# Kernel optimization log

Hardware: AMD Instinct MI355X
Metric: run time of the kernel (lower is better)

The kernel has to match this reference:

```python
import jax, jax.numpy as jnp
import numpy as np


def setup_inputs() -> dict:
    key = jax.random.key(0)
    ks = jax.random.split(key, 8)
    B, D, S, H, W = 32, 256, 64, 64, 64
    L = H * W
    return {
        "x": jax.random.normal(ks[0], (B, D, L), jnp.float32),
        "H": H,
        "W": W,
        "w_bcdt": jax.random.normal(ks[1], (3 * S, D), jnp.float32) * 0.02,
        "b_bcdt": jnp.zeros((3 * S,), jnp.float32),
        "w_dw": jax.random.normal(ks[2], (3 * S, 1, 3, 3), jnp.float32) * 0.1,
        "b_dw": jnp.zeros((3 * S,), jnp.float32),
        "w_hz": jax.random.normal(ks[3], (2 * D, D), jnp.float32) * 0.02,
        "b_hz": jnp.zeros((2 * D,), jnp.float32),
        "w_out": jax.random.normal(ks[4], (D, D), jnp.float32) * 0.02,
        "b_out": jnp.zeros((D,), jnp.float32),
        "A_param": jax.random.uniform(ks[5], (S,), jnp.float32, minval=1.0, maxval=16.0),
        "D_param": jnp.ones((1,), jnp.float32),
    }


def reference(x, H, W, w_bcdt, b_bcdt, w_dw, b_dw, w_hz, b_hz, w_out, b_out, A_param, D_param):
    batch, d_model, L = x.shape
    S = A_param.shape[0]
    # BCdt_proj: pointwise conv1d -> (B, 3S, L)
    bcdt = jnp.einsum('oc,bcl->bol', w_bcdt, x) + b_bcdt[None, :, None]
    # depthwise 3x3 conv over (H, W)
    x4 = bcdt.reshape(batch, 3 * S, H, W)
    x4 = jax.lax.conv_general_dilated(
        x4, w_dw, window_strides=(1, 1), padding=((1, 1), (1, 1)),
        dimension_numbers=('NCHW', 'OIHW', 'NCHW'), feature_group_count=3 * S,
    ) + b_dw[None, :, None, None]
    bcdt = x4.reshape(batch, 3 * S, L)
    Bm, Cm, dt = jnp.split(bcdt, 3, axis=1)  # each (B, S, L)
    # gating: softmax over sequence dim L
    Aw = jax.nn.softmax(dt + A_param[None, :, None], axis=-1)
    AB = Aw * Bm  # (B, S, L)
    # global state compression: h = x @ AB^T -> (B, d_model, S)
    h = jnp.einsum('bdl,bsl->bds', x, AB)
    # hz_proj (pointwise conv1d over length S)
    hz = jnp.einsum('oc,bcs->bos', w_hz, h) + b_hz[None, :, None]
    h2, z = jnp.split(hz, 2, axis=1)  # each (B, d_inner, S)
    g = h2 * jax.nn.silu(z) + h2 * D_param[0]
    hout = jnp.einsum('oc,bcs->bos', w_out, g) + b_out[None, :, None]  # (B, d_model, S)
    # expand back: y = h @ C -> (B, d_model, L)
    y = jnp.einsum('bds,bsl->bdl', hout, Cm).reshape(batch, d_model, H, W)
    return (y, hout)
```

## Files before the change

### kernel.cpp

```cpp
#include <hip/hip_runtime.h>
#include <math.h>

#define B_  32
#define D_  256
#define L_  4096
#define S_  64
#define C3_ 192

#define YSZ    ((size_t)B_ * D_ * L_)
#define HOUTSZ ((size_t)B_ * D_ * S_)
#define NCHUNK 16

typedef __attribute__((ext_vector_type(8))) short short8;
typedef __attribute__((ext_vector_type(4))) float f32x4;

__device__ __forceinline__ short f2bf(float f) {
    unsigned u = __float_as_uint(f);
    u += 0x7fffu + ((u >> 16) & 1u);
    return (short)(u >> 16);
}

__device__ __forceinline__ short8 ld_cvt8(const float* p) {
    const float4* q = reinterpret_cast<const float4*>(p);
    float4 p0 = q[0], p1 = q[1];
    short8 s;
    s[0] = f2bf(p0.x); s[1] = f2bf(p0.y); s[2] = f2bf(p0.z); s[3] = f2bf(p0.w);
    s[4] = f2bf(p1.x); s[5] = f2bf(p1.y); s[6] = f2bf(p1.z); s[7] = f2bf(p1.w);
    return s;
}

__global__ __launch_bounds__(256) void k1_bcdt_mfma(
    const float* __restrict__ x, const float* __restrict__ w,
    const float* __restrict__ bias, float* __restrict__ out)
{
    __shared__ __align__(16) short A_lds[192][40];
    __shared__ __align__(16) short B_lds[128][40];
    const int l0 = blockIdx.x * 128;
    const int b  = blockIdx.y;
    const int tid  = threadIdx.x;
    const int lane = tid & 63;
    const int wv   = tid >> 6;
    const int lm   = lane & 15;
    const int kg   = lane >> 4;
    const float* xb = x + (size_t)b * D_ * L_;

    f32x4 acc[12][2];
    #pragma unroll
    for (int mi = 0; mi < 12; ++mi)
        #pragma unroll
        for (int nj = 0; nj < 2; ++nj)
            acc[mi][nj] = (f32x4){0.f, 0.f, 0.f, 0.f};

    for (int k0 = 0; k0 < D_; k0 += 32) {
        if (k0) __syncthreads();
        #pragma unroll
        for (int q = 0; q < 3; ++q) {
            int task = q * 256 + tid;
            int o = task >> 2, kk = (task & 3) * 8;
            *(short8*)&A_lds[o][kk] = ld_cvt8(w + (size_t)o * D_ + k0 + kk);
        }
        #pragma unroll
        for (int q = 0; q < 2; ++q) {
            int task = q * 256 + tid;
            int l = task & 127, dg = task >> 7;
            const float* xp = xb + (size_t)(k0 + dg * 8) * L_ + l0 + l;
            short8 s;
            #pragma unroll
            for (int r = 0; r < 8; ++r) s[r] = f2bf(xp[(size_t)r * L_]);
            *(short8*)&B_lds[l][dg * 8] = s;
        }
        __syncthreads();
        short8 bb[2];
        #pragma unroll
        for (int nj = 0; nj < 2; ++nj)
            bb[nj] = *(const short8*)&B_lds[wv * 32 + nj * 16 + lm][kg * 8];
        #pragma unroll
        for (int mi = 0; mi < 12; ++mi) {
            short8 a = *(const short8*)&A_lds[mi * 16 + lm][kg * 8];
            #pragma unroll
            for (int nj = 0; nj < 2; ++nj)
                acc[mi][nj] = __builtin_amdgcn_mfma_f32_16x16x32_bf16(
                    a, bb[nj], acc[mi][nj], 0, 0, 0);
        }
    }
    float* ob = out + (size_t)b * C3_ * L_;
    const int col = l0 + wv * 32 + lm;
    #pragma unroll
    for (int mi = 0; mi < 12; ++mi) {
        #pragma unroll
        for (int r = 0; r < 4; ++r) {
            int o = mi * 16 + kg * 4 + r;
            float bv = bias[o];
            #pragma unroll
            for (int nj = 0; nj < 2; ++nj)
                ob[(size_t)o * L_ + col + nj * 16] = acc[mi][nj][r] + bv;
        }
    }
}

__global__ __launch_bounds__(256) void k2a_conv_cm(
    const float* __restrict__ pre, const float* __restrict__ wdw,
    const float* __restrict__ bdw, float* __restrict__ cm)
{
    __shared__ float sm[66][66];
    const int s = blockIdx.x;
    const int b = blockIdx.y;
    const int c = 64 + s;
    const int tid = threadIdx.x;
    for (int i = tid; i < 66 * 66; i += 256) (&sm[0][0])[i] = 0.f;
    __syncthreads();
    const float* ip = pre + ((size_t)b * C3_ + c) * L_;
    for (int p = tid; p < 4096; p += 256)
        sm[(p >> 6) + 1][(p & 63) + 1] = ip[p];
    __syncthreads();
    const float* wp = wdw + c * 9;
    float w00 = wp[0], w01 = wp[1], w02 = wp[2],
          w10 = wp[3], w11 = wp[4], w12 = wp[5],
          w20 = wp[6], w21 = wp[7], w22 = wp[8];
    float bb = bdw[c];
    float* op = cm + ((size_t)b * S_ + s) * L_;
    for (int p = tid; p < 4096; p += 256) {
        int yy = p >> 6, xx = p & 63;
        op[p] = bb
            + sm[yy][xx] * w00     + sm[yy][xx + 1] * w01     + sm[yy][xx + 2] * w02
            + sm[yy + 1][xx] * w10 + sm[yy + 1][xx + 1] * w11 + sm[yy + 1][xx + 2] * w12
            + sm[yy + 2][xx] * w20 + sm[yy + 2][xx + 1] * w21 + sm[yy + 2][xx + 2] * w22;
    }
}

__global__ __launch_bounds__(256) void k2b_softmax_ab(
    const float* __restrict__ pre, const float* __restrict__ wdw,
    const float* __restrict__ bdw, float* __restrict__ ab)
{
    __shared__ float sm[66][66];
    __shared__ float red[4];
    const int s = blockIdx.x;
    const int b = blockIdx.y;
    const int tid = threadIdx.x;
    for (int i = tid; i < 66 * 66; i += 256) (&sm[0][0])[i] = 0.f;
    __syncthreads();
    const int cd = 128 + s;
    {
        const float* ip = pre + ((size_t)b * C3_ + cd) * L_;
        for (int p = tid; p < 4096; p += 256)
            sm[(p >> 6) + 1][(p & 63) + 1] = ip[p];
    }
    __syncthreads();
    float dt[16];
    {
        const float* wp = wdw + cd * 9;
        float w00 = wp[0], w01 = wp[1], w02 = wp[2],
              w10 = wp[3], w11 = wp[4], w12 = wp[5],
              w20 = wp[6], w21 = wp[7], w22 = wp[8];
        float bb = bdw[cd];
        #pragma unroll
        for (int i = 0; i < 16; ++i) {
            int p = tid + 256 * i;
            int yy = p >> 6, xx = p & 63;
            dt[i] = bb
                + sm[yy][xx] * w00     + sm[yy][xx + 1] * w01     + sm[yy][xx + 2] * w02
                + sm[yy + 1][xx] * w10 + sm[yy + 1][xx + 1] * w11 + sm[yy + 1][xx + 2] * w12
                + sm[yy + 2][xx] * w20 + sm[yy + 2][xx + 1] * w21 + sm[yy + 2][xx + 2] * w22;
        }
    }
    float mx = dt[0];
    #pragma unroll
    for (int i = 1; i < 16; ++i) mx = fmaxf(mx, dt[i]);
    #pragma unroll
    for (int off = 32; off >= 1; off >>= 1) mx = fmaxf(mx, __shfl_xor(mx, off, 64));
    if ((tid & 63) == 0) red[tid >> 6] = mx;
    __syncthreads();
    mx = fmaxf(fmaxf(red[0], red[1]), fmaxf(red[2], red[3]));
    float e[16];
    float lsum = 0.f;
    #pragma unroll
    for (int i = 0; i < 16; ++i) { e[i] = expf(dt[i] - mx); lsum += e[i]; }
    #pragma unroll
    for (int off = 32; off >= 1; off >>= 1) lsum += __shfl_xor(lsum, off, 64);
    __syncthreads();
    if ((tid & 63) == 0) red[tid >> 6] = lsum;
    __syncthreads();
    const float inv = 1.f / (red[0] + red[1] + red[2] + red[3]);
    {
        const float* ip = pre + ((size_t)b * C3_ + s) * L_;
        for (int p = tid; p < 4096; p += 256)
            sm[(p >> 6) + 1][(p & 63) + 1] = ip[p];
    }
    __syncthreads();
    {
        const float* wp = wdw + s * 9;
        float w00 = wp[0], w01 = wp[1], w02 = wp[2],
              w10 = wp[3], w11 = wp[4], w12 = wp[5],
              w20 = wp[6], w21 = wp[7], w22 = wp[8];
        float bb = bdw[s];
        float* op = ab + ((size_t)b * S_ + s) * L_;
        #pragma unroll
        for (int i = 0; i < 16; ++i) {
            int p = tid + 256 * i;
            int yy = p >> 6, xx = p & 63;
            float bm = bb
                + sm[yy][xx] * w00     + sm[yy][xx + 1] * w01     + sm[yy][xx + 2] * w02
                + sm[yy + 1][xx] * w10 + sm[yy + 1][xx + 1] * w11 + sm[yy + 1][xx + 2] * w12
                + sm[yy + 2][xx] * w20 + sm[yy + 2][xx + 1] * w21 + sm[yy + 2][xx + 2] * w22;
            op[p] = e[i] * inv * bm;
        }
    }
}

__global__ __launch_bounds__(256) void k3_hpart_mfma(
    const float* __restrict__ x, const float* __restrict__ ab,
    float* __restrict__ hp)
{
    const int dt    = blockIdx.x;
    const int b     = blockIdx.y;
    const int chunk = blockIdx.z;
    const int tid  = threadIdx.x;
    const int lane = tid & 63;
    const int wv   = tid >> 6;
    const int wr   = wv >> 1, wc = wv & 1;
    const int lm   = lane & 15, kg = lane >> 4;
    const int d_base = dt * 128 + wr * 64;
    const int s_base = wc * 32;
    const float* xb  = x  + (size_t)b * D_ * L_;
    const float* abb = ab + (size_t)b * S_ * L_;

    f32x4 acc[4][2];
    #pragma unroll
    for (int mi = 0; mi < 4; ++mi)
        #pragma unroll
        for (int nj = 0; nj < 2; ++nj)
            acc[mi][nj] = (f32x4){0.f, 0.f, 0.f, 0.f};

    #pragma unroll 2
    for (int ks = 0; ks < 8; ++ks) {
        const int l = chunk * 256 + ks * 32 + kg * 8;
        short8 bfr[2];
        #pragma unroll
        for (int nj = 0; nj < 2; ++nj)
            bfr[nj] = ld_cvt8(abb + (size_t)(s_base + nj * 16 + lm) * L_ + l);
        #pragma unroll
        for (int mi = 0; mi < 4; ++mi) {
            short8 a = ld_cvt8(xb + (size_t)(d_base + mi * 16 + lm) * L_ + l);
            #pragma unroll
            for (int nj = 0; nj < 2; ++nj)
                acc[mi][nj] = __builtin_amdgcn_mfma_f32_16x16x32_bf16(
                    a, bfr[nj], acc[mi][nj], 0, 0, 0);
        }
    }
    float* hpo = hp + (size_t)chunk * HOUTSZ + (size_t)b * D_ * S_;
    #pragma unroll
    for (int mi = 0; mi < 4; ++mi)
        #pragma unroll
        for (int r = 0; r < 4; ++r) {
            int d = d_base + mi * 16 + kg * 4 + r;
            #pragma unroll
            for (int nj = 0; nj < 2; ++nj)
                hpo[(size_t)d * S_ + s_base + nj * 16 + lm] = acc[mi][nj][r];
        }
}

__global__ __launch_bounds__(256) void k3r_reduce(
    const float* __restrict__ hp, float* __restrict__ h)
{
    size_t i = (size_t)blockIdx.x * 256 + threadIdx.x;
    float sum = 0.f;
    #pragma unroll
    for (int c = 0; c < NCHUNK; ++c) sum += hp[(size_t)c * HOUTSZ + i];
    h[i] = sum;
}

__global__ __launch_bounds__(256) void k4a_gate(
    const float* __restrict__ h, const float* __restrict__ whz,
    const float* __restrict__ bhz, const float* __restrict__ Dp,
    float* __restrict__ g)
{
    __shared__ float Ah[16][68];
    __shared__ float Az[16][68];
    __shared__ float Bs[16][64];
    const int o0 = blockIdx.x * 64;
    const int b  = blockIdx.y;
    const int tid = threadIdx.x;
    const int tx = tid & 15, ty = tid >> 4;
    float acch[4][4] = {}, accz[4][4] = {};
    const float* hb = h + (size_t)b * D_ * S_;
    for (int k0 = 0; k0 < D_; k0 += 16) {
        {
            int o = tid & 15, k = tid >> 4;
            #pragma unroll
            for (int i = 0; i < 4; ++i) {
                Ah[k][o + 16 * i] = whz[(size_t)(o0 + o + 16 * i) * D_ + k0 + k];
                Az[k][o + 16 * i] = whz[(size_t)(o0 + o + 16 * i + 256) * D_ + k0 + k];
            }
        }
        {
            int s = tid & 63, k = tid >> 6;
            #pragma unroll
            for (int i = 0; i < 4; ++i)
                Bs[k + 4 * i][s] = hb[(size_t)(k0 + k + 4 * i) * S_ + s];
        }
        __syncthreads();
        #pragma unroll
        for (int k = 0; k < 16; ++k) {
            float ah[4], az[4], bb[4];
            #pragma unroll
            for (int i = 0; i < 4; ++i) { ah[i] = Ah[k][ty * 4 + i]; az[i] = Az[k][ty * 4 + i]; }
            #pragma unroll
            for (int j = 0; j < 4; ++j) bb[j] = Bs[k][tx * 4 + j];
            #pragma unroll
            for (int i = 0; i < 4; ++i)
                #pragma unroll
                for (int j = 0; j < 4; ++j) {
                    acch[i][j] += ah[i] * bb[j];
                    accz[i][j] += az[i] * bb[j];
                }
        }
        __syncthreads();
    }
    const float dp = Dp[0];
    #pragma unroll
    for (int i = 0; i < 4; ++i) {
        int o = o0 + ty * 4 + i;
        float bh = bhz[o], bz = bhz[o + 256];
        #pragma unroll
        for (int j = 0; j < 4; ++j) {
            float h2 = acch[i][j] + bh;
            float z  = accz[i][j] + bz;
            float sil = z / (1.f + expf(-z));
            g[((size_t)b * D_ + o) * S_ + tx * 4 + j] = h2 * (sil + dp);
        }
    }
}

__global__ __launch_bounds__(256) void k4b_hout(
    const float* __restrict__ g, const float* __restrict__ wout,
    const float* __restrict__ bout, float* __restrict__ hout)
{
    __shared__ float At[16][68];
    __shared__ float Bs[16][64];
    const int o0 = blockIdx.x * 64;
    const int b  = blockIdx.y;
    const int tid = threadIdx.x;
    const int tx = tid & 15, ty = tid >> 4;
    float acc[4][4] = {};
    const float* gb = g + (size_t)b * D_ * S_;
    for (int k0 = 0; k0 < D_; k0 += 16) {
        {
            int o = tid & 15, k = tid >> 4;
            #pragma unroll
            for (int i = 0; i < 4; ++i)
                At[k][o + 16 * i] = wout[(size_t)(o0 + o + 16 * i) * D_ + k0 + k];
        }
        {
            int s = tid & 63, k = tid >> 6;
            #pragma unroll
            for (int i = 0; i < 4; ++i)
                Bs[k + 4 * i][s] = gb[(size_t)(k0 + k + 4 * i) * S_ + s];
        }
        __syncthreads();
        #pragma unroll
        for (int k = 0; k < 16; ++k) {
            float a[4], bb[4];
            #pragma unroll
            for (int i = 0; i < 4; ++i) a[i] = At[k][ty * 4 + i];
            #pragma unroll
            for (int j = 0; j < 4; ++j) bb[j] = Bs[k][tx * 4 + j];
            #pragma unroll
            for (int i = 0; i < 4; ++i)
                #pragma unroll
                for (int j = 0; j < 4; ++j)
                    acc[i][j] += a[i] * bb[j];
        }
        __syncthreads();
    }
    #pragma unroll
    for (int i = 0; i < 4; ++i) {
        int o = o0 + ty * 4 + i;
        float bv = bout[o];
        #pragma unroll
        for (int j = 0; j < 4; ++j)
            hout[((size_t)b * D_ + o) * S_ + tx * 4 + j] = acc[i][j] + bv;
    }
}

__global__ __launch_bounds__(256) void k5_expand_mfma(
    const float* __restrict__ hout, const float* __restrict__ cm,
    float* __restrict__ y)
{
    __shared__ __align__(16) short A_lds[64][72];
    __shared__ __align__(16) short B_lds[128][72];
    const int l0 = blockIdx.x * 128;
    const int d0 = blockIdx.y * 64;
    const int b  = blockIdx.z;
    const int tid  = threadIdx.x;
    const int lane = tid & 63;
    const int wv   = tid >> 6;
    const int lm   = lane & 15, kg = lane >> 4;

    #pragma unroll
    for (int q = 0; q < 2; ++q) {
        int task = q * 256 + tid;
        int d = task >> 3, sg = (task & 7) * 8;
        *(short8*)&A_lds[d][sg] = ld_cvt8(hout + ((size_t)b * D_ + d0 + d) * S_ + sg);
    }
    #pragma unroll
    for (int q = 0; q < 4; ++q) {
        int l = tid & 127;
        int sg = (q * 2 + (tid >> 7)) * 8;
        const float* cp = cm + ((size_t)b * S_ + sg) * L_ + l0 + l;
        short8 s;
        #pragma unroll
        for (int r = 0; r < 8; ++r) s[r] = f2bf(cp[(size_t)r * L_]);
        *(short8*)&B_lds[l][sg] = s;
    }
    __syncthreads();

    f32x4 acc[4][2];
    #pragma unroll
    for (int mi = 0; mi < 4; ++mi)
        #pragma unroll
        for (int nj = 0; nj < 2; ++nj)
            acc[mi][nj] = (f32x4){0.f, 0.f, 0.f, 0.f};
    #pragma unroll
    for (int ks = 0; ks < 2; ++ks) {
        short8 bb[2];
        #pragma unroll
        for (int nj = 0; nj < 2; ++nj)
            bb[nj] = *(const short8*)&B_lds[wv * 32 + nj * 16 + lm][ks * 32 + kg * 8];
        #pragma unroll
        for (int mi = 0; mi < 4; ++mi) {
            short8 a = *(const short8*)&A_lds[mi * 16 + lm][ks * 32 + kg * 8];
            #pragma unroll
            for (int nj = 0; nj < 2; ++nj)
                acc[mi][nj] = __builtin_amdgcn_mfma_f32_16x16x32_bf16(
                    a, bb[nj], acc[mi][nj], 0, 0, 0);
        }
    }
    const int col = l0 + wv * 32 + lm;
    #pragma unroll
    for (int mi = 0; mi < 4; ++mi)
        #pragma unroll
        for (int r = 0; r < 4; ++r)
            #pragma unroll
            for (int nj = 0; nj < 2; ++nj)
                y[((size_t)b * D_ + d0 + mi * 16 + kg * 4 + r) * L_ + col + nj * 16]
                    = acc[mi][nj][r];
}

extern "C" void kernel_launch(void* const* d_in, const int* in_sizes, int n_in,
                              void* d_out, int out_size, void* d_ws, size_t ws_size,
                              hipStream_t stream)
{
    const float* x      = (const float*)d_in[0];
    const float* w_bcdt = (const float*)d_in[3];
    const float* b_bcdt = (const float*)d_in[4];
    const float* w_dw   = (const float*)d_in[5];
    const float* b_dw   = (const float*)d_in[6];
    const float* w_hz   = (const float*)d_in[7];
    const float* b_hz   = (const float*)d_in[8];
    const float* w_out  = (const float*)d_in[9];
    const float* b_out  = (const float*)d_in[10];
    const float* Dp     = (const float*)d_in[12];

    float* ws  = (float*)d_ws;
    float* pre = ws;
    float* ab  = ws + 25165824;
    float* cm  = ab + 8388608;
    float* hp  = pre;
    float* h   = pre + 8388608;
    float* g   = pre + 8388608 + 524288;

    float* y    = (float*)d_out;
    float* hout = (float*)d_out + YSZ;

    k1_bcdt_mfma  <<<dim3(32, 32),     256, 0, stream>>>(x, w_bcdt, b_bcdt, pre);
    k2a_conv_cm   <<<dim3(64, 32),     256, 0, stream>>>(pre, w_dw, b_dw, cm);
    k2b_softmax_ab<<<dim3(64, 32),     256, 0, stream>>>(pre, w_dw, b_dw, ab);
    k3_hpart_mfma <<<dim3(2, 32, NCHUNK), 256, 0, stream>>>(x, ab, hp);
    k3r_reduce    <<<2048,             256, 0, stream>>>(hp, h);
    k4a_gate      <<<dim3(4, 32),      256, 0, stream>>>(h, w_hz, b_hz, Dp, g);
    k4b_hout      <<<dim3(4, 32),      256, 0, stream>>>(g, w_out, b_out, hout);
    k5_expand_mfma<<<dim3(32, 4, 32),  256, 0, stream>>>(hout, cm, y);
}
```

Baseline: 256.1 us.

## Store intermediates in bf16, merge conv kernels, fold chunk reduction into gate

The pre-projection, Cm and AB intermediates are now written and read as bf16 instead of fp32, which halves their memory traffic. The downstream MFMA kernels can then load bf16 directly without converting. The two depthwise-conv kernels are merged into one launch that splits by block index. The separate chunk-reduction kernel is removed, and k4a_gate sums the partial results while loading. This costs some precision in the intermediates and adds redundant partial-sum reads inside the gate kernel.

```diff
diff --git a/kernel.cpp b/kernel.cpp
--- a/kernel.cpp
+++ b/kernel.cpp
@@ -13,13 +13,17 @@
 
 typedef __attribute__((ext_vector_type(8))) short short8;
 typedef __attribute__((ext_vector_type(4))) float f32x4;
+typedef unsigned short ushort_t;
+typedef unsigned int uint_t;
 
 __device__ __forceinline__ short f2bf(float f) {
     unsigned u = __float_as_uint(f);
     u += 0x7fffu + ((u >> 16) & 1u);
     return (short)(u >> 16);
 }
-
+__device__ __forceinline__ float bf2f(ushort_t u) {
+    return __uint_as_float((uint_t)u << 16);
+}
 __device__ __forceinline__ short8 ld_cvt8(const float* p) {
     const float4* q = reinterpret_cast<const float4*>(p);
     float4 p0 = q[0], p1 = q[1];
@@ -31,7 +35,7 @@
 
 __global__ __launch_bounds__(256) void k1_bcdt_mfma(
     const float* __restrict__ x, const float* __restrict__ w,
-    const float* __restrict__ bias, float* __restrict__ out)
+    const float* __restrict__ bias, ushort_t* __restrict__ out)
 {
     __shared__ __align__(16) short A_lds[192][40];
     __shared__ __align__(16) short B_lds[128][40];
@@ -83,7 +87,7 @@
                     a, bb[nj], acc[mi][nj], 0, 0, 0);
         }
     }
-    float* ob = out + (size_t)b * C3_ * L_;
+    ushort_t* ob = out + (size_t)b * C3_ * L_;
     const int col = l0 + wv * 32 + lm;
     #pragma unroll
     for (int mi = 0; mi < 12; ++mi) {
@@ -93,57 +97,65 @@
             float bv = bias[o];
             #pragma unroll
             for (int nj = 0; nj < 2; ++nj)
-                ob[(size_t)o * L_ + col + nj * 16] = acc[mi][nj][r] + bv;
-        }
-    }
-}
-
-__global__ __launch_bounds__(256) void k2a_conv_cm(
-    const float* __restrict__ pre, const float* __restrict__ wdw,
-    const float* __restrict__ bdw, float* __restrict__ cm)
-{
-    __shared__ float sm[66][66];
-    const int s = blockIdx.x;
-    const int b = blockIdx.y;
-    const int c = 64 + s;
-    const int tid = threadIdx.x;
-    for (int i = tid; i < 66 * 66; i += 256) (&sm[0][0])[i] = 0.f;
-    __syncthreads();
-    const float* ip = pre + ((size_t)b * C3_ + c) * L_;
-    for (int p = tid; p < 4096; p += 256)
-        sm[(p >> 6) + 1][(p & 63) + 1] = ip[p];
-    __syncthreads();
-    const float* wp = wdw + c * 9;
-    float w00 = wp[0], w01 = wp[1], w02 = wp[2],
-          w10 = wp[3], w11 = wp[4], w12 = wp[5],
-          w20 = wp[6], w21 = wp[7], w22 = wp[8];
-    float bb = bdw[c];
-    float* op = cm + ((size_t)b * S_ + s) * L_;
-    for (int p = tid; p < 4096; p += 256) {
-        int yy = p >> 6, xx = p & 63;
-        op[p] = bb
-            + sm[yy][xx] * w00     + sm[yy][xx + 1] * w01     + sm[yy][xx + 2] * w02
-            + sm[yy + 1][xx] * w10 + sm[yy + 1][xx + 1] * w11 + sm[yy + 1][xx + 2] * w12
-            + sm[yy + 2][xx] * w20 + sm[yy + 2][xx + 1] * w21 + sm[yy + 2][xx + 2] * w22;
-    }
-}
-
-__global__ __launch_bounds__(256) void k2b_softmax_ab(
-    const float* __restrict__ pre, const float* __restrict__ wdw,
-    const float* __restrict__ bdw, float* __restrict__ ab)
+                ob[(size_t)o * L_ + col + nj * 16] =
+                    (ushort_t)f2bf(acc[mi][nj][r] + bv);
+        }
+    }
+}
+
+__global__ __launch_bounds__(256) void k2_conv(
+    const ushort_t* __restrict__ pre, const float* __restrict__ wdw,
+    const float* __restrict__ bdw, ushort_t* __restrict__ cm,
+    ushort_t* __restrict__ ab)
 {
     __shared__ float sm[66][66];
     __shared__ float red[4];
-    const int s = blockIdx.x;
-    const int b = blockIdx.y;
+    const int t   = blockIdx.x;
+    const int b   = blockIdx.y;
+    const int s   = t & 63;
     const int tid = threadIdx.x;
+
     for (int i = tid; i < 66 * 66; i += 256) (&sm[0][0])[i] = 0.f;
     __syncthreads();
+
+    if (t < 64) {
+        const int c = 64 + s;
+        const uint_t* ip32 = reinterpret_cast<const uint_t*>(
+            pre + ((size_t)b * C3_ + c) * L_);
+        for (int p2 = tid; p2 < 2048; p2 += 256) {
+            uint_t v = ip32[p2];
+            int q = p2 * 2;
+            sm[(q >> 6) + 1][(q & 63) + 1] = bf2f((ushort_t)(v & 0xffffu));
+            sm[(q >> 6) + 1][(q & 63) + 2] = bf2f((ushort_t)(v >> 16));
+        }
+        __syncthreads();
+        const float* wp = wdw + c * 9;
+        float w00 = wp[0], w01 = wp[1], w02 = wp[2],
+              w10 = wp[3], w11 = wp[4], w12 = wp[5],
+              w20 = wp[6], w21 = wp[7], w22 = wp[8];
+        float bb = bdw[c];
+        ushort_t* op = cm + ((size_t)b * S_ + s) * L_;
+        for (int p = tid; p < 4096; p += 256) {
+            int yy = p >> 6, xx = p & 63;
+            float v = bb
+                + sm[yy][xx] * w00     + sm[yy][xx + 1] * w01     + sm[yy][xx + 2] * w02
+                + sm[yy + 1][xx] * w10 + sm[yy + 1][xx + 1] * w11 + sm[yy + 1][xx + 2] * w12
+                + sm[yy + 2][xx] * w20 + sm[yy + 2][xx + 1] * w21 + sm[yy + 2][xx + 2] * w22;
+            op[p] = (ushort_t)f2bf(v);
+        }
+        return;
+    }
+
     const int cd = 128 + s;
     {
-        const float* ip = pre + ((size_t)b * C3_ + cd) * L_;
-        for (int p = tid; p < 4096; p += 256)
-            sm[(p >> 6) + 1][(p & 63) + 1] = ip[p];
+        const uint_t* ip32 = reinterpret_cast<const uint_t*>(
+            pre + ((size_t)b * C3_ + cd) * L_);
+        for (int p2 = tid; p2 < 2048; p2 += 256) {
+            uint_t v = ip32[p2];
+            int q = p2 * 2;
+            sm[(q >> 6) + 1][(q & 63) + 1] = bf2f((ushort_t)(v & 0xffffu));
+            sm[(q >> 6) + 1][(q & 63) + 2] = bf2f((ushort_t)(v >> 16));
+        }
     }
     __syncthreads();
     float dt[16];
@@ -182,9 +194,14 @@
     __syncthreads();
     const float inv = 1.f / (red[0] + red[1] + red[2] + red[3]);
     {
-        const float* ip = pre + ((size_t)b * C3_ + s) * L_;
-        for (int p = tid; p < 4096; p += 256)
-            sm[(p >> 6) + 1][(p & 63) + 1] = ip[p];
+        const uint_t* ip32 = reinterpret_cast<const uint_t*>(
+            pre + ((size_t)b * C3_ + s) * L_);
+        for (int p2 = tid; p2 < 2048; p2 += 256) {
+            uint_t v = ip32[p2];
+            int q = p2 * 2;
+            sm[(q >> 6) + 1][(q & 63) + 1] = bf2f((ushort_t)(v & 0xffffu));
+            sm[(q >> 6) + 1][(q & 63) + 2] = bf2f((ushort_t)(v >> 16));
+        }
     }
     __syncthreads();
     {
@@ -193,7 +210,7 @@
               w10 = wp[3], w11 = wp[4], w12 = wp[5],
               w20 = wp[6], w21 = wp[7], w22 = wp[8];
         float bb = bdw[s];
-        float* op = ab + ((size_t)b * S_ + s) * L_;
+        ushort_t* op = ab + ((size_t)b * S_ + s) * L_;
         #pragma unroll
         for (int i = 0; i < 16; ++i) {
             int p = tid + 256 * i;
@@ -202,13 +219,13 @@
                 + sm[yy][xx] * w00     + sm[yy][xx + 1] * w01     + sm[yy][xx + 2] * w02
                 + sm[yy + 1][xx] * w10 + sm[yy + 1][xx + 1] * w11 + sm[yy + 1][xx + 2] * w12
                 + sm[yy + 2][xx] * w20 + sm[yy + 2][xx + 1] * w21 + sm[yy + 2][xx + 2] * w22;
-            op[p] = e[i] * inv * bm;
+            op[p] = (ushort_t)f2bf(e[i] * inv * bm);
         }
     }
 }
 
 __global__ __launch_bounds__(256) void k3_hpart_mfma(
-    const float* __restrict__ x, const float* __restrict__ ab,
+    const float* __restrict__ x, const ushort_t* __restrict__ ab,
     float* __restrict__ hp)
 {
     const int dt    = blockIdx.x;
@@ -221,8 +238,8 @@
     const int lm   = lane & 15, kg = lane >> 4;
     const int d_base = dt * 128 + wr * 64;
     const int s_base = wc * 32;
-    const float* xb  = x  + (size_t)b * D_ * L_;
-    const float* abb = ab + (size_t)b * S_ * L_;
+    const float*    xb  = x  + (size_t)b * D_ * L_;
+    const ushort_t* abb = ab + (size_t)b * S_ * L_;
 
     f32x4 acc[4][2];
     #pragma unroll
@@ -237,7 +254,8 @@
         short8 bfr[2];
         #pragma unroll
         for (int nj = 0; nj < 2; ++nj)
-            bfr[nj] = ld_cvt8(abb + (size_t)(s_base + nj * 16 + lm) * L_ + l);
+            bfr[nj] = *reinterpret_cast<const short8*>(
+                abb + (size_t)(s_base + nj * 16 + lm) * L_ + l);
         #pragma unroll
         for (int mi = 0; mi < 4; ++mi) {
             short8 a = ld_cvt8(xb + (size_t)(d_base + mi * 16 + lm) * L_ + l);
@@ -259,18 +277,8 @@
         }
 }
 
-__global__ __launch_bounds__(256) void k3r_reduce(
-    const float* __restrict__ hp, float* __restrict__ h)
-{
-    size_t i = (size_t)blockIdx.x * 256 + threadIdx.x;
-    float sum = 0.f;
-    #pragma unroll
-    for (int c = 0; c < NCHUNK; ++c) sum += hp[(size_t)c * HOUTSZ + i];
-    h[i] = sum;
-}
-
 __global__ __launch_bounds__(256) void k4a_gate(
-    const float* __restrict__ h, const float* __restrict__ whz,
+    const float* __restrict__ hp, const float* __restrict__ whz,
     const float* __restrict__ bhz, const float* __restrict__ Dp,
     float* __restrict__ g)
 {
@@ -282,7 +290,7 @@
     const int tid = threadIdx.x;
     const int tx = tid & 15, ty = tid >> 4;
     float acch[4][4] = {}, accz[4][4] = {};
-    const float* hb = h + (size_t)b * D_ * S_;
+    const float* hb = hp + (size_t)b * D_ * S_;
     for (int k0 = 0; k0 < D_; k0 += 16) {
         {
             int o = tid & 15, k = tid >> 4;
@@ -295,8 +303,13 @@
         {
             int s = tid & 63, k = tid >> 6;
             #pragma unroll
-            for (int i = 0; i < 4; ++i)
-                Bs[k + 4 * i][s] = hb[(size_t)(k0 + k + 4 * i) * S_ + s];
+            for (int i = 0; i < 4; ++i) {
+                float sum = 0.f;
+                #pragma unroll
+                for (int c = 0; c < NCHUNK; ++c)
+                    sum += hb[(size_t)c * HOUTSZ + (size_t)(k0 + k + 4 * i) * S_ + s];
+                Bs[k + 4 * i][s] = sum;
+            }
         }
         __syncthreads();
         #pragma unroll
@@ -383,7 +396,7 @@
 }
 
 __global__ __launch_bounds__(256) void k5_expand_mfma(
-    const float* __restrict__ hout, const float* __restrict__ cm,
+    const float* __restrict__ hout, const ushort_t* __restrict__ cm,
     float* __restrict__ y)
 {
     __shared__ __align__(16) short A_lds[64][72];
@@ -406,10 +419,10 @@
     for (int q = 0; q < 4; ++q) {
         int l = tid & 127;
         int sg = (q * 2 + (tid >> 7)) * 8;
-        const float* cp = cm + ((size_t)b * S_ + sg) * L_ + l0 + l;
+        const ushort_t* cp = cm + ((size_t)b * S_ + sg) * L_ + l0 + l;
         short8 s;
         #pragma unroll
-        for (int r = 0; r < 8; ++r) s[r] = f2bf(cp[(size_t)r * L_]);
+        for (int r = 0; r < 8; ++r) s[r] = (short)cp[(size_t)r * L_];
         *(short8*)&B_lds[l][sg] = s;
     }
     __syncthreads();
@@ -461,23 +474,20 @@
     const float* b_out  = (const float*)d_in[10];
     const float* Dp     = (const float*)d_in[12];
 
-    float* ws  = (float*)d_ws;
-    float* pre = ws;
-    float* ab  = ws + 25165824;
-    float* cm  = ab + 8388608;
-    float* hp  = pre;
-    float* h   = pre + 8388608;
-    float* g   = pre + 8388608 + 524288;
+    char* base = (char*)d_ws;
+    ushort_t* pre_bf = (ushort_t*)(base);
+    ushort_t* ab_bf  = (ushort_t*)(base + 50331648);
+    ushort_t* cm_bf  = (ushort_t*)(base + 67108864);
+    float*    hp     = (float*)   (base + 83886080);
+    float*    g      = (float*)   (base + 117440512);
 
     float* y    = (float*)d_out;
     float* hout = (float*)d_out + YSZ;
 
-    k1_bcdt_mfma  <<<dim3(32, 32),     256, 0, stream>>>(x, w_bcdt, b_bcdt, pre);
-    k2a_conv_cm   <<<dim3(64, 32),     256, 0, stream>>>(pre, w_dw, b_dw, cm);
-    k2b_softmax_ab<<<dim3(64, 32),     256, 0, stream>>>(pre, w_dw, b_dw, ab);
-    k3_hpart_mfma <<<dim3(2, 32, NCHUNK), 256, 0, stream>>>(x, ab, hp);
-    k3r_reduce    <<<2048,             256, 0, stream>>>(hp, h);
-    k4a_gate      <<<dim3(4, 32),      256, 0, stream>>>(h, w_hz, b_hz, Dp, g);
-    k4b_hout      <<<dim3(4, 32),      256, 0, stream>>>(g, w_out, b_out, hout);
-    k5_expand_mfma<<<dim3(32, 4, 32),  256, 0, stream>>>(hout, cm, y);
-}
+    k1_bcdt_mfma  <<<dim3(32, 32),        256, 0, stream>>>(x, w_bcdt, b_bcdt, pre_bf);
+    k2_conv       <<<dim3(128, 32),       256, 0, stream>>>(pre_bf, w_dw, b_dw, cm_bf, ab_bf);
+    k3_hpart_mfma <<<dim3(2, 32, NCHUNK), 256, 0, stream>>>(x, ab_bf, hp);
+    k4a_gate      <<<dim3(4, 32),         256, 0, stream>>>(hp, w_hz, b_hz, Dp, g);
+    k4b_hout      <<<dim3(4, 32),         256, 0, stream>>>(g, w_out, b_out, hout);
+    k5_expand_mfma<<<dim3(32, 4, 32),     256, 0, stream>>>(hout, cm_bf, y);
+}
```

After: 221.0 us. -13.7%, faster.
